# Kernel optimization log

Hardware: AMD Instinct MI355X
Metric: run time of the kernel (lower is better)

The kernel has to match this reference:

```python
import jax, jax.numpy as jnp
import numpy as np

DIMS = [2000, 256, 64, 32, 10]
N = 4096
BN_EPS = 1e-5
ALPHA = 1.0  # forward calls cal_latent(hidden, 1); ClusterlingLayer default alpha=1


def _xavier(k, out_d, in_d):
    lim = float(np.sqrt(6.0 / (in_d + out_d)))
    return jax.random.uniform(k, (out_d, in_d), minval=-lim, maxval=lim, dtype=jnp.float32)


def setup_inputs() -> dict:
    key = jax.random.key(0)
    ks = jax.random.split(key, 6)
    d0, d1, d2, d3, k_clusters = DIMS
    return {
        "x": jax.random.normal(ks[0], (N, d0), dtype=jnp.float32),
        "W0": _xavier(ks[1], d1, d0), "b0": jnp.zeros((d1,), jnp.float32),
        "g0": jnp.ones((d1,), jnp.float32), "beta0": jnp.zeros((d1,), jnp.float32),
        "W1": _xavier(ks[2], d2, d1), "b1": jnp.zeros((d2,), jnp.float32),
        "g1": jnp.ones((d2,), jnp.float32), "beta1": jnp.zeros((d2,), jnp.float32),
        "W2": _xavier(ks[3], d3, d2), "b2": jnp.zeros((d3,), jnp.float32),
        "centers": _xavier(ks[4], k_clusters, d3),
    }


def _bn(h, g, b):
    # BatchNorm1d in training mode: biased batch statistics
    mu = jnp.mean(h, axis=0)
    var = jnp.mean((h - mu) ** 2, axis=0)
    return g * (h - mu) * jax.lax.rsqrt(var + BN_EPS) + b


def reference(x, W0, b0, g0, beta0, W1, b1, g1, beta1, W2, b2, centers):
    # ----- encoder: Linear+BN+ReLU blocks, last Linear bare -----
    h = jax.nn.relu(_bn(x @ W0.T + b0, g0, beta0))
    h = jax.nn.relu(_bn(h @ W1.T + b1, g1, beta1))
    latent = h @ W2.T + b2                       # [N, d_latent]

    # ----- F.normalize(latent, dim=1) -----
    normalized = latent / jnp.maximum(
        jnp.linalg.norm(latent, axis=1, keepdims=True), 1e-12)

    # ----- ClusterlingLayer: Student-t soft assignment to centers -----
    d2c = jnp.sum((latent[:, None, :] - centers[None, :, :]) ** 2, axis=-1)  # [N, K]
    x1 = 1.0 + d2c / ALPHA
    qc = 1.0 / x1
    latent_dist1 = qc / jnp.sum(qc, axis=1, keepdims=True)
    latent_dist2 = x1

    # ----- cal_latent(latent, alpha=1): N x N Student-t affinity -----
    sum_y = jnp.sum(latent * latent, axis=1)     # [N]
    num = -2.0 * (latent @ latent.T) + sum_y[:, None] + sum_y[None, :]  # sq. dists
    num = (1.0 + num / ALPHA) ** (-(ALPHA + 1.0) / 2.0)                 # [N, N]
    diag = jnp.diag(jnp.diagonal(num))
    zerodiag = num - diag
    latent_p = zerodiag / jnp.sum(zerodiag, axis=1, keepdims=True)

    # ----- target_dis: p^2 with two row-normalizations -----
    latent_q = latent_p ** 2 / jnp.sum(latent_p, axis=1, keepdims=True)
    latent_q = latent_q / jnp.sum(latent_q, axis=1, keepdims=True)

    latent_p = latent_p + diag
    latent_q = latent_q + diag

    return (latent, latent_dist1, latent_dist2, latent_q, latent_p, num, normalized)
```

## Files before the change

kernel.cpp:

```cpp
#include <hip/hip_runtime.h>

#define NR 4096
#define BN_EPS 1e-5f

#define OFF_LATENT 0
#define OFF_D1     131072
#define OFF_D2     172032
#define OFF_Q      212992
#define OFF_P      16990208
#define OFF_NUM    33767424
#define OFF_NORM   50544640

#define WS_SUM0   0
#define WS_SQ0    256
#define WS_SUM1   512
#define WS_SQ1    576
#define WS_ROWSUM 640
#define WS_ZERO_F 4736
#define WS_DIAG   4736
#define WS_SUMY   8832

__global__ void zero_ws(float* __restrict__ ws) {
    int i = blockIdx.x * blockDim.x + threadIdx.x;
    if (i < WS_ZERO_F) ws[i] = 0.0f;
}

__global__ void h0_init(float* __restrict__ H0, const float* __restrict__ b0) {
    int i4 = blockIdx.x * blockDim.x + threadIdx.x;
    ((float4*)H0)[i4] = ((const float4*)b0)[i4 & 63];
}

__global__ __launch_bounds__(256) void gemm_splitk_128x64(
    const float* __restrict__ A, const float* __restrict__ B,
    float* __restrict__ C, int lda, int ldb, int ldc, int kc)
{
    __shared__ float As[16][128];
    __shared__ float Bs[16][64];
    const int t  = threadIdx.x;
    const int tx = t & 15;
    const int ty = t >> 4;
    const int i0 = blockIdx.x * 128;
    const int n0 = blockIdx.y * 64;
    const int kb = blockIdx.z * kc;

    const int ra  = t >> 1;
    const int ka  = (t & 1) * 8;
    const int rb  = t >> 2;
    const int kbq = (t & 3) * 4;

    float acc[8][4] = {};

    for (int kt = 0; kt < kc; kt += 16) {
        float4 a0 = *(const float4*)&A[(size_t)(i0 + ra) * lda + kb + kt + ka];
        float4 a1 = *(const float4*)&A[(size_t)(i0 + ra) * lda + kb + kt + ka + 4];
        float4 b0 = *(const float4*)&B[(size_t)(n0 + rb) * ldb + kb + kt + kbq];
        __syncthreads();
        As[ka+0][ra] = a0.x; As[ka+1][ra] = a0.y; As[ka+2][ra] = a0.z; As[ka+3][ra] = a0.w;
        As[ka+4][ra] = a1.x; As[ka+5][ra] = a1.y; As[ka+6][ra] = a1.z; As[ka+7][ra] = a1.w;
        Bs[kbq+0][rb] = b0.x; Bs[kbq+1][rb] = b0.y; Bs[kbq+2][rb] = b0.z; Bs[kbq+3][rb] = b0.w;
        __syncthreads();
        #pragma unroll
        for (int k = 0; k < 16; ++k) {
            float4 av0 = *(const float4*)&As[k][ty*8];
            float4 av1 = *(const float4*)&As[k][ty*8+4];
            float4 bv  = *(const float4*)&Bs[k][tx*4];
            float am[8] = {av0.x,av0.y,av0.z,av0.w,av1.x,av1.y,av1.z,av1.w};
            float bb[4] = {bv.x,bv.y,bv.z,bv.w};
            #pragma unroll
            for (int m = 0; m < 8; ++m)
                #pragma unroll
                for (int n = 0; n < 4; ++n)
                    acc[m][n] = fmaf(am[m], bb[n], acc[m][n]);
        }
    }
    #pragma unroll
    for (int m = 0; m < 8; ++m)
        #pragma unroll
        for (int n = 0; n < 4; ++n)
            atomicAdd(&C[(size_t)(i0 + ty*8 + m) * ldc + n0 + tx*4 + n], acc[m][n]);
}

__global__ __launch_bounds__(256) void gemm_bias_64x64(
    const float* __restrict__ A, const float* __restrict__ B,
    const float* __restrict__ bias, float* __restrict__ C,
    int lda, int ldb, int ldc, int K)
{
    __shared__ float As[16][64];
    __shared__ float Bs[16][64];
    const int t  = threadIdx.x;
    const int tx = t & 15, ty = t >> 4;
    const int i0 = blockIdx.x * 64;
    const int n0 = blockIdx.y * 64;
    const int r  = t >> 2;
    const int kq = (t & 3) * 4;

    float acc[4][4] = {};

    for (int kt = 0; kt < K; kt += 16) {
        float4 a4 = *(const float4*)&A[(size_t)(i0 + r) * lda + kt + kq];
        float4 b4 = *(const float4*)&B[(size_t)(n0 + r) * ldb + kt + kq];
        __syncthreads();
        As[kq+0][r] = a4.x; As[kq+1][r] = a4.y; As[kq+2][r] = a4.z; As[kq+3][r] = a4.w;
        Bs[kq+0][r] = b4.x; Bs[kq+1][r] = b4.y; Bs[kq+2][r] = b4.z; Bs[kq+3][r] = b4.w;
        __syncthreads();
        #pragma unroll
        for (int k = 0; k < 16; ++k) {
            float4 av = *(const float4*)&As[k][ty*4];
            float4 bv = *(const float4*)&Bs[k][tx*4];
            float am[4] = {av.x,av.y,av.z,av.w};
            float bb[4] = {bv.x,bv.y,bv.z,bv.w};
            #pragma unroll
            for (int m = 0; m < 4; ++m)
                #pragma unroll
                for (int n = 0; n < 4; ++n)
                    acc[m][n] = fmaf(am[m], bb[n], acc[m][n]);
        }
    }
    float4 bz = *(const float4*)&bias[n0 + tx*4];
    #pragma unroll
    for (int m = 0; m < 4; ++m) {
        float4 o;
        o.x = acc[m][0] + bz.x; o.y = acc[m][1] + bz.y;
        o.z = acc[m][2] + bz.z; o.w = acc[m][3] + bz.w;
        *(float4*)&C[(size_t)(i0 + ty*4 + m) * ldc + n0 + tx*4] = o;
    }
}

__global__ void bn_stats(const float* __restrict__ H, float* __restrict__ sum,
                         float* __restrict__ sumsq, int cols)
{
    const int t = threadIdx.x;
    const int col = t & (cols - 1);
    const int sub = t / cols;
    const int rstep = 256 / cols;
    const int rbase = blockIdx.x * 64;
    float s = 0.f, sq = 0.f;
    for (int r = sub; r < 64; r += rstep) {
        float v = H[(size_t)(rbase + r) * cols + col];
        s += v; sq += v * v;
    }
    atomicAdd(&sum[col], s);
    atomicAdd(&sumsq[col], sq);
}

__global__ void bn_relu(float* __restrict__ H, const float* __restrict__ sum,
                        const float* __restrict__ sumsq, const float* __restrict__ g,
                        const float* __restrict__ beta, int cols)
{
    int i4 = blockIdx.x * blockDim.x + threadIdx.x;
    float4 v = ((const float4*)H)[i4];
    int c0 = (i4 * 4) & (cols - 1);
    float o[4] = {v.x, v.y, v.z, v.w};
    #pragma unroll
    for (int e = 0; e < 4; ++e) {
        int c = c0 + e;
        float mu  = sum[c]   * (1.0f / 4096.0f);
        float var = sumsq[c] * (1.0f / 4096.0f) - mu * mu;
        float xn = (o[e] - mu) / sqrtf(var + BN_EPS);
        o[e] = fmaxf(g[c] * xn + beta[c], 0.0f);
    }
    ((float4*)H)[i4] = make_float4(o[0], o[1], o[2], o[3]);
}

__global__ __launch_bounds__(256) void latent_kernel(
    const float* __restrict__ H1, const float* __restrict__ W2,
    const float* __restrict__ b2, const float* __restrict__ centers,
    float* __restrict__ out_latent, float* __restrict__ out_norm,
    float* __restrict__ out_d1, float* __restrict__ out_d2,
    float* __restrict__ sumy)
{
    __shared__ float W2T[64][32];
    __shared__ float cent[320];
    __shared__ float b2s[32];
    __shared__ float Hs[8][64];
    const int t = threadIdx.x;
    {
        int c = t >> 3, dd = (t & 7) * 8;
        #pragma unroll
        for (int q = 0; q < 8; ++q) W2T[dd + q][c] = W2[c * 64 + dd + q];
    }
    for (int c = t; c < 320; c += 256) cent[c] = centers[c];
    if (t < 32) b2s[t] = b2[t];
    const int base = blockIdx.x * 8;
    if (t < 128) {
        int rr = t >> 4, off = (t & 15) * 4;
        *(float4*)&Hs[rr][off] = *(const float4*)&H1[(size_t)(base + rr) * 64 + off];
    }
    __syncthreads();

    const int g = t >> 5, lane = t & 31;
    const int row = base + g;
    float acc = b2s[lane];
    #pragma unroll
    for (int d = 0; d < 64; ++d) acc = fmaf(Hs[g][d], W2T[d][lane], acc);
    out_latent[(size_t)row * 32 + lane] = acc;

    float ss = acc * acc;
    #pragma unroll
    for (int off = 16; off; off >>= 1) ss += __shfl_xor(ss, off);
    float denom = fmaxf(sqrtf(ss), 1e-12f);
    out_norm[(size_t)row * 32 + lane] = acc / denom;
    if (lane == 0) sumy[row] = ss;

    float qsum = 0.f, myx1 = 0.f, myqc = 0.f;
    #pragma unroll
    for (int k = 0; k < 10; ++k) {
        float dv = acc - cent[k * 32 + lane];
        float sq = dv * dv;
        #pragma unroll
        for (int off = 16; off; off >>= 1) sq += __shfl_xor(sq, off);
        float x1 = 1.0f + sq;
        float qc = 1.0f / x1;
        qsum += qc;
        if (lane == k) { myx1 = x1; myqc = qc; }
    }
    if (lane < 10) {
        out_d2[row * 10 + lane] = myx1;
        out_d1[row * 10 + lane] = myqc / qsum;
    }
}

__global__ __launch_bounds__(256) void num_kernel(
    const float* __restrict__ latent, const float* __restrict__ sumy,
    float* __restrict__ num_out, float* __restrict__ rowsum, float* __restrict__ diagv)
{
    __shared__ float Li[128][36];
    __shared__ float Lj[128][36];
    __shared__ float scr[128];
    const int t  = threadIdx.x;
    const int i0 = blockIdx.x * 128;
    const int j0 = blockIdx.y * 128;
    {
        int r = t & 127;
        const float* src = (t < 128) ? &latent[(size_t)(i0 + r) * 32]
                                     : &latent[(size_t)(j0 + r) * 32];
        float (*dst)[36] = (t < 128) ? Li : Lj;
        #pragma unroll
        for (int q = 0; q < 8; ++q)
            *(float4*)&dst[r][q * 4] = *(const float4*)&src[q * 4];
    }
    __syncthreads();

    const int tx = t & 15, ty = t >> 4;
    float acc[8][8] = {};
    #pragma unroll
    for (int d4 = 0; d4 < 8; ++d4) {
        float4 bv[8];
        #pragma unroll
        for (int n = 0; n < 8; ++n) bv[n] = *(const float4*)&Lj[tx + 16*n][d4*4];
        #pragma unroll
        for (int m = 0; m < 8; ++m) {
            float4 av = *(const float4*)&Li[ty + 16*m][d4*4];
            #pragma unroll
            for (int n = 0; n < 8; ++n) {
                acc[m][n] = fmaf(av.x, bv[n].x, acc[m][n]);
                acc[m][n] = fmaf(av.y, bv[n].y, acc[m][n]);
                acc[m][n] = fmaf(av.z, bv[n].z, acc[m][n]);
                acc[m][n] = fmaf(av.w, bv[n].w, acc[m][n]);
            }
        }
    }
    float syi[8], syj[8];
    #pragma unroll
    for (int m = 0; m < 8; ++m) syi[m] = sumy[i0 + ty + 16*m];
    #pragma unroll
    for (int n = 0; n < 8; ++n) syj[n] = sumy[j0 + tx + 16*n];

    float racc[8] = {};
    #pragma unroll
    for (int m = 0; m < 8; ++m) {
        const int i = i0 + ty + 16*m;
        #pragma unroll
        for (int n = 0; n < 8; ++n) {
            const int j = j0 + tx + 16*n;
            float sq = syi[m] + syj[n] - 2.0f * acc[m][n];
            float v = 1.0f / (1.0f + sq);
            num_out[(size_t)i * NR + j] = v;
            racc[m] += v;
            if (i == j) diagv[i] = v;
        }
    }
    __syncthreads();
    if (t < 128) scr[t] = 0.f;
    __syncthreads();
    #pragma unroll
    for (int m = 0; m < 8; ++m) atomicAdd(&scr[ty + 16*m], racc[m]);
    __syncthreads();
    if (t < 128) atomicAdd(&rowsum[i0 + t], scr[t]);
}

__global__ __launch_bounds__(256) void pq_kernel(
    const float* __restrict__ num, const float* __restrict__ rowsum,
    const float* __restrict__ diagv, float* __restrict__ p_out,
    float* __restrict__ q_out)
{
    const int i = blockIdx.x;
    const int t = threadIdx.x;
    const float dg = diagv[i];
    const float inv_S1 = 1.0f / (rowsum[i] - dg);
    const float* nrow = &num[(size_t)i * NR];
    float* prow = &p_out[(size_t)i * NR];
    float* qrow = &q_out[(size_t)i * NR];

    float pr[16];
    float s = 0.f, s2 = 0.f;
    #pragma unroll
    for (int it = 0; it < 4; ++it) {
        int j4 = it * 256 + t;
        float4 v = ((const float4*)nrow)[j4];
        float vv[4] = {v.x, v.y, v.z, v.w};
        #pragma unroll
        for (int e = 0; e < 4; ++e) {
            int j = j4 * 4 + e;
            float p = (j == i) ? 0.0f : vv[e] * inv_S1;
            pr[it * 4 + e] = p;
            s += p; s2 += p * p;
        }
        ((float4*)prow)[j4] = make_float4(
            (j4*4+0 == i) ? dg : pr[it*4+0], (j4*4+1 == i) ? dg : pr[it*4+1],
            (j4*4+2 == i) ? dg : pr[it*4+2], (j4*4+3 == i) ? dg : pr[it*4+3]);
    }
    #pragma unroll
    for (int off = 32; off; off >>= 1) {
        s  += __shfl_xor(s, off);
        s2 += __shfl_xor(s2, off);
    }
    __shared__ float rA[4], rB[4];
    const int wid = t >> 6;
    if ((t & 63) == 0) { rA[wid] = s; rB[wid] = s2; }
    __syncthreads();
    const float sp  = rA[0] + rA[1] + rA[2] + rA[3];
    const float sp2 = rB[0] + rB[1] + rB[2] + rB[3];
    const float inv_sp   = 1.0f / sp;
    const float inv_sumq = sp / sp2;
    #pragma unroll
    for (int it = 0; it < 4; ++it) {
        int j4 = it * 256 + t;
        float qv[4];
        #pragma unroll
        for (int e = 0; e < 4; ++e) {
            int j = j4 * 4 + e;
            float p = pr[it * 4 + e];
            qv[e] = (j == i) ? dg : (p * p * inv_sp) * inv_sumq;
        }
        ((float4*)qrow)[j4] = make_float4(qv[0], qv[1], qv[2], qv[3]);
    }
}

extern "C" void kernel_launch(void* const* d_in, const int* in_sizes, int n_in,
                              void* d_out, int out_size, void* d_ws, size_t ws_size,
                              hipStream_t stream) {
    const float* x       = (const float*)d_in[0];
    const float* W0      = (const float*)d_in[1];
    const float* b0      = (const float*)d_in[2];
    const float* g0      = (const float*)d_in[3];
    const float* beta0   = (const float*)d_in[4];
    const float* W1      = (const float*)d_in[5];
    const float* b1      = (const float*)d_in[6];
    const float* g1      = (const float*)d_in[7];
    const float* beta1   = (const float*)d_in[8];
    const float* W2      = (const float*)d_in[9];
    const float* b2      = (const float*)d_in[10];
    const float* centers = (const float*)d_in[11];
    float* out = (float*)d_out;
    float* ws  = (float*)d_ws;

    float* H0 = out + OFF_Q;
    float* H1 = out + OFF_Q + 4096 * 256;

    zero_ws<<<19, 256, 0, stream>>>(ws);

    h0_init<<<1024, 256, 0, stream>>>(H0, b0);
    gemm_splitk_128x64<<<dim3(32, 4, 5), 256, 0, stream>>>(x, W0, H0, 2000, 2000, 256, 400);
    bn_stats<<<64, 256, 0, stream>>>(H0, ws + WS_SUM0, ws + WS_SQ0, 256);
    bn_relu<<<1024, 256, 0, stream>>>(H0, ws + WS_SUM0, ws + WS_SQ0, g0, beta0, 256);

    gemm_bias_64x64<<<dim3(64, 1), 256, 0, stream>>>(H0, W1, b1, H1, 256, 256, 64, 256);
    bn_stats<<<64, 256, 0, stream>>>(H1, ws + WS_SUM1, ws + WS_SQ1, 64);
    bn_relu<<<256, 256, 0, stream>>>(H1, ws + WS_SUM1, ws + WS_SQ1, g1, beta1, 64);

    latent_kernel<<<512, 256, 0, stream>>>(H1, W2, b2, centers,
        out + OFF_LATENT, out + OFF_NORM, out + OFF_D1, out + OFF_D2, ws + WS_SUMY);

    num_kernel<<<dim3(32, 32), 256, 0, stream>>>(out + OFF_LATENT, ws + WS_SUMY,
        out + OFF_NUM, ws + WS_ROWSUM, ws + WS_DIAG);

    pq_kernel<<<4096, 256, 0, stream>>>(out + OFF_NUM, ws + WS_ROWSUM, ws + WS_DIAG,
        out + OFF_P, out + OFF_Q);
}
```

Measured before the change: 502.1 us.

## Prefetch next K tile in split-K GEMM, reuse it for layer 1, widen BN stats

The split-K GEMM now loads the next global K tile into registers before computing on the current shared-memory tile, so global latency overlaps with the FMAs. The second linear layer drops its dedicated 64x64 GEMM in favour of the split-K kernel (4 K-splits with atomics), with a generalized bias-init kernel run first. bn_stats launches four times as many blocks over fewer rows each, trading more parallelism for more atomic traffic. Split-K for layer 1 also adds atomic contention and a separate init launch.

```diff
diff --git a/kernel.cpp b/kernel.cpp
--- a/kernel.cpp
+++ b/kernel.cpp
@@ -25,9 +25,9 @@
     if (i < WS_ZERO_F) ws[i] = 0.0f;
 }
 
-__global__ void h0_init(float* __restrict__ H0, const float* __restrict__ b0) {
+__global__ void h_init(float* __restrict__ H, const float* __restrict__ bias, int cols4) {
     int i4 = blockIdx.x * blockDim.x + threadIdx.x;
-    ((float4*)H0)[i4] = ((const float4*)b0)[i4 & 63];
+    ((float4*)H)[i4] = ((const float4*)bias)[i4 & (cols4 - 1)];
 }
 
 __global__ __launch_bounds__(256) void gemm_splitk_128x64(
@@ -48,17 +48,26 @@
     const int rb  = t >> 2;
     const int kbq = (t & 3) * 4;
 
+    const float* pA = &A[(size_t)(i0 + ra) * lda + kb + ka];
+    const float* pB = &B[(size_t)(n0 + rb) * ldb + kb + kbq];
+
     float acc[8][4] = {};
 
+    float4 a0 = *(const float4*)(pA);
+    float4 a1 = *(const float4*)(pA + 4);
+    float4 b0 = *(const float4*)(pB);
+
     for (int kt = 0; kt < kc; kt += 16) {
-        float4 a0 = *(const float4*)&A[(size_t)(i0 + ra) * lda + kb + kt + ka];
-        float4 a1 = *(const float4*)&A[(size_t)(i0 + ra) * lda + kb + kt + ka + 4];
-        float4 b0 = *(const float4*)&B[(size_t)(n0 + rb) * ldb + kb + kt + kbq];
         __syncthreads();
         As[ka+0][ra] = a0.x; As[ka+1][ra] = a0.y; As[ka+2][ra] = a0.z; As[ka+3][ra] = a0.w;
         As[ka+4][ra] = a1.x; As[ka+5][ra] = a1.y; As[ka+6][ra] = a1.z; As[ka+7][ra] = a1.w;
         Bs[kbq+0][rb] = b0.x; Bs[kbq+1][rb] = b0.y; Bs[kbq+2][rb] = b0.z; Bs[kbq+3][rb] = b0.w;
         __syncthreads();
+        if (kt + 16 < kc) {
+            a0 = *(const float4*)(pA + kt + 16);
+            a1 = *(const float4*)(pA + kt + 20);
+            b0 = *(const float4*)(pB + kt + 16);
+        }
         #pragma unroll
         for (int k = 0; k < 16; ++k) {
             float4 av0 = *(const float4*)&As[k][ty*8];
@@ -80,52 +89,6 @@
             atomicAdd(&C[(size_t)(i0 + ty*8 + m) * ldc + n0 + tx*4 + n], acc[m][n]);
 }
 
-__global__ __launch_bounds__(256) void gemm_bias_64x64(
-    const float* __restrict__ A, const float* __restrict__ B,
-    const float* __restrict__ bias, float* __restrict__ C,
-    int lda, int ldb, int ldc, int K)
-{
-    __shared__ float As[16][64];
-    __shared__ float Bs[16][64];
-    const int t  = threadIdx.x;
-    const int tx = t & 15, ty = t >> 4;
-    const int i0 = blockIdx.x * 64;
-    const int n0 = blockIdx.y * 64;
-    const int r  = t >> 2;
-    const int kq = (t & 3) * 4;
-
-    float acc[4][4] = {};
-
-    for (int kt = 0; kt < K; kt += 16) {
-        float4 a4 = *(const float4*)&A[(size_t)(i0 + r) * lda + kt + kq];
-        float4 b4 = *(const float4*)&B[(size_t)(n0 + r) * ldb + kt + kq];
-        __syncthreads();
-        As[kq+0][r] = a4.x; As[kq+1][r] = a4.y; As[kq+2][r] = a4.z; As[kq+3][r] = a4.w;
-        Bs[kq+0][r] = b4.x; Bs[kq+1][r] = b4.y; Bs[kq+2][r] = b4.z; Bs[kq+3][r] = b4.w;
-        __syncthreads();
-        #pragma unroll
-        for (int k = 0; k < 16; ++k) {
-            float4 av = *(const float4*)&As[k][ty*4];
-            float4 bv = *(const float4*)&Bs[k][tx*4];
-            float am[4] = {av.x,av.y,av.z,av.w};
-            float bb[4] = {bv.x,bv.y,bv.z,bv.w};
-            #pragma unroll
-            for (int m = 0; m < 4; ++m)
-                #pragma unroll
-                for (int n = 0; n < 4; ++n)
-                    acc[m][n] = fmaf(am[m], bb[n], acc[m][n]);
-        }
-    }
-    float4 bz = *(const float4*)&bias[n0 + tx*4];
-    #pragma unroll
-    for (int m = 0; m < 4; ++m) {
-        float4 o;
-        o.x = acc[m][0] + bz.x; o.y = acc[m][1] + bz.y;
-        o.z = acc[m][2] + bz.z; o.w = acc[m][3] + bz.w;
-        *(float4*)&C[(size_t)(i0 + ty*4 + m) * ldc + n0 + tx*4] = o;
-    }
-}
-
 __global__ void bn_stats(const float* __restrict__ H, float* __restrict__ sum,
                          float* __restrict__ sumsq, int cols)
 {
@@ -133,9 +96,9 @@
     const int col = t & (cols - 1);
     const int sub = t / cols;
     const int rstep = 256 / cols;
-    const int rbase = blockIdx.x * 64;
+    const int rbase = blockIdx.x * 16;
     float s = 0.f, sq = 0.f;
-    for (int r = sub; r < 64; r += rstep) {
+    for (int r = sub; r < 16; r += rstep) {
         float v = H[(size_t)(rbase + r) * cols + col];
         s += v; sq += v * v;
     }
@@ -370,13 +333,14 @@
 
     zero_ws<<<19, 256, 0, stream>>>(ws);
 
-    h0_init<<<1024, 256, 0, stream>>>(H0, b0);
+    h_init<<<1024, 256, 0, stream>>>(H0, b0, 64);
     gemm_splitk_128x64<<<dim3(32, 4, 5), 256, 0, stream>>>(x, W0, H0, 2000, 2000, 256, 400);
-    bn_stats<<<64, 256, 0, stream>>>(H0, ws + WS_SUM0, ws + WS_SQ0, 256);
+    bn_stats<<<256, 256, 0, stream>>>(H0, ws + WS_SUM0, ws + WS_SQ0, 256);
     bn_relu<<<1024, 256, 0, stream>>>(H0, ws + WS_SUM0, ws + WS_SQ0, g0, beta0, 256);
 
-    gemm_bias_64x64<<<dim3(64, 1), 256, 0, stream>>>(H0, W1, b1, H1, 256, 256, 64, 256);
-    bn_stats<<<64, 256, 0, stream>>>(H1, ws + WS_SUM1, ws + WS_SQ1, 64);
+    h_init<<<256, 256, 0, stream>>>(H1, b1, 16);
+    gemm_splitk_128x64<<<dim3(32, 1, 4), 256, 0, stream>>>(H0, W1, H1, 256, 256, 64, 64);
+    bn_stats<<<256, 256, 0, stream>>>(H1, ws + WS_SUM1, ws + WS_SQ1, 64);
     bn_relu<<<256, 256, 0, stream>>>(H1, ws + WS_SUM1, ws + WS_SQ1, g1, beta1, 64);
 
     latent_kernel<<<512, 256, 0, stream>>>(H1, W2, b2, centers,
```

Result: slower. 517.3 us (+3.0%).
